# Optimization experiments

Measured on AMD Instinct MI355X. Metric: run time of the kernel, lower is better.

## Reference

```python
import jax, jax.numpy as jnp
import numpy as np

B, S, H = 4, 2048, 1024
NH, HD = 16, 64


def setup_inputs() -> dict:
    key = jax.random.key(0)
    ks = jax.random.split(key, 5)
    scale = 1.0 / np.sqrt(H)
    x = jax.random.normal(ks[0], (B, S, H), dtype=jnp.float32)
    w_qkv = jax.random.normal(ks[1], (H, 3 * H), dtype=jnp.float32) * scale
    b_qkv = jnp.zeros((3 * H,), dtype=jnp.float32)
    w_out = jax.random.normal(ks[2], (H, H), dtype=jnp.float32) * scale
    b_out = jnp.zeros((H,), dtype=jnp.float32)
    return {"x": x, "w_qkv": w_qkv, "b_qkv": b_qkv, "w_out": w_out, "b_out": b_out}


def reference(x, w_qkv, b_qkv, w_out, b_out):
    bsz, seq_len, hidden = x.shape
    qkv = x @ w_qkv + b_qkv  # [B,S,3H]
    q, k, v = jnp.split(qkv, 3, axis=-1)

    def heads(t):
        return t.reshape(bsz, seq_len, NH, HD).transpose(0, 2, 1, 3)  # [B,NH,S,HD]

    q, k, v = heads(q), heads(k), heads(v)
    scale = HD ** (-0.5)
    attn = jnp.einsum("bhqd,bhkd->bhqk", q, k) * scale  # [B,NH,S,S]
    causal = jnp.tril(jnp.ones((seq_len, seq_len), dtype=bool))
    attn = jnp.where(causal, attn, -jnp.inf)
    probs = jax.nn.softmax(attn, axis=-1)
    out = jnp.einsum("bhqk,bhkd->bhqd", probs, v)
    out = out.transpose(0, 2, 1, 3).reshape(bsz, seq_len, hidden)
    return out @ w_out + b_out
```

## Files before the change

### kernel.cpp

```cpp
#include <hip/hip_runtime.h>
#include <hip/hip_bf16.h>
#include <cstdint>

#define B_  4
#define S_  2048
#define H_  1024
#define NH_ 16
#define HD_ 64

using short8  = __attribute__((ext_vector_type(8))) short;
using floatx4 = __attribute__((ext_vector_type(4))) float;

__device__ __forceinline__ unsigned short f2b(float f) {
  union { float f; unsigned int u; } x; x.f = f;
  unsigned int r = x.u + 0x7fffu + ((x.u >> 16) & 1u);
  return (unsigned short)(r >> 16);
}
__device__ __forceinline__ unsigned short f2b_fast(float f) {
  union { float f; unsigned int u; } x; x.f = f;
  return (unsigned short)((x.u + 0x8000u) >> 16);
}
__device__ __forceinline__ unsigned int pack2(float a, float b) {
  return (unsigned int)f2b(a) | ((unsigned int)f2b(b) << 16);
}

__device__ __forceinline__ void async16(void* lds, const void* g) {
  __builtin_amdgcn_global_load_lds(
      (const __attribute__((address_space(1))) unsigned int*)g,
      (__attribute__((address_space(3))) unsigned int*)lds, 16, 0, 0);
}

__global__ void k_convert(const float* __restrict__ in, unsigned short* __restrict__ out, int n) {
  int i = (blockIdx.x * blockDim.x + threadIdx.x) * 4;
  if (i >= n) return;
  float4 v = *(const float4*)(in + i);
  ushort4 o;
  o.x = f2b(v.x); o.y = f2b(v.y); o.z = f2b(v.z); o.w = f2b(v.w);
  *(ushort4*)(out + i) = o;
}

__global__ void k_transpose_convert(const float* __restrict__ in, unsigned short* __restrict__ out,
                                    int R, int C) {
  __shared__ float tile[32][33];
  int tx = threadIdx.x & 31, ty = threadIdx.x >> 5;
  int c0 = blockIdx.x * 32, r0 = blockIdx.y * 32;
  for (int i = 0; i < 4; i++) {
    int r = r0 + ty + i * 8;
    tile[ty + i * 8][tx] = in[(size_t)r * C + c0 + tx];
  }
  __syncthreads();
  for (int i = 0; i < 4; i++) {
    int c = c0 + ty + i * 8;
    out[(size_t)c * R + r0 + tx] = f2b(tile[tx][ty + i * 8]);
  }
}

template <bool OUT_BF16>
__global__ __launch_bounds__(256, 2) void k_gemm_bt(
    const unsigned short* __restrict__ A,
    const unsigned short* __restrict__ BT,
    const float* __restrict__ bias,
    void* __restrict__ Cout,
    unsigned short* __restrict__ vt,
    int M, int N, int K) {
  __shared__ __align__(16) unsigned short As[2][128 * 64];
  __shared__ __align__(16) unsigned short Bs[2][128 * 64];
  const int tid  = threadIdx.x;
  const int lane = tid & 63, wave = tid >> 6;
  const int quad = lane >> 4, l16 = lane & 15;
  const int wm = wave >> 1, wn = wave & 1;
  const int m0 = blockIdx.y * 128, n0 = blockIdx.x * 128;
  const int wv2 = wave & 1;

  const unsigned short* srcbase = (wave < 2) ? A : BT;
  const int base0 = (wave < 2) ? m0 : n0;

  floatx4 acc[4][4];
  for (int mt = 0; mt < 4; mt++)
    for (int nt = 0; nt < 4; nt++)
      acc[mt][nt] = (floatx4){0.f, 0.f, 0.f, 0.f};

  auto stage = [&](int k0, int bufi) {
    unsigned short* dst = (wave < 2) ? &As[bufi][0] : &Bs[bufi][0];
    for (int j = 0; j < 8; j++) {
      int c = wv2 * 512 + j * 64 + lane;
      int row = c >> 3, slot = c & 7;
      int c8 = slot ^ (row & 7);
      async16(&dst[c * 8], &srcbase[(size_t)(base0 + row) * K + k0 + c8 * 8]);
    }
  };

  stage(0, 0);
  int it = 0;
  for (int k0 = 0; k0 < K; k0 += 64, it++) {
    const int cur = it & 1;
    __syncthreads();
    if (k0 + 64 < K) stage(k0 + 64, cur ^ 1);
    for (int kh = 0; kh < 2; kh++) {
      short8 af[4], bq[4];
      for (int t = 0; t < 4; t++) {
        int ra = wm * 64 + t * 16 + l16;
        int rb = wn * 64 + t * 16 + l16;
        af[t] = *(const short8*)&As[cur][(ra * 8 + ((kh * 4 + quad) ^ (ra & 7))) * 8];
        bq[t] = *(const short8*)&Bs[cur][(rb * 8 + ((kh * 4 + quad) ^ (rb & 7))) * 8];
      }
      for (int mt = 0; mt < 4; mt++)
        for (int nt = 0; nt < 4; nt++)
          acc[mt][nt] = __builtin_amdgcn_mfma_f32_16x16x32_bf16(af[mt], bq[nt], acc[mt][nt], 0, 0, 0);
    }
  }

  if (OUT_BF16 && n0 >= 2048) {
    for (int mt = 0; mt < 4; mt++) {
      int row0 = m0 + wm * 64 + mt * 16 + quad * 4;
      int b = row0 >> 11, s = row0 & 2047;
      for (int nt = 0; nt < 4; nt++) {
        int col = n0 + wn * 64 + nt * 16 + l16;
        float bv = bias[col];
        uint2 u;
        u.x = pack2(acc[mt][nt][0] + bv, acc[mt][nt][1] + bv);
        u.y = pack2(acc[mt][nt][2] + bv, acc[mt][nt][3] + bv);
        *(uint2*)&vt[(size_t)(b * 1024 + (col - 2048)) * S_ + s] = u;
      }
    }
  } else {
    for (int mt = 0; mt < 4; mt++) {
      int row = m0 + wm * 64 + mt * 16 + quad * 4;
      for (int nt = 0; nt < 4; nt++) {
        int col = n0 + wn * 64 + nt * 16 + l16;
        float bv = bias[col];
        for (int r = 0; r < 4; r++) {
          float v = acc[mt][nt][r] + bv;
          if (OUT_BF16) ((unsigned short*)Cout)[(size_t)(row + r) * N + col] = f2b(v);
          else          ((float*)Cout)[(size_t)(row + r) * N + col] = v;
        }
      }
    }
  }
}

__global__ __launch_bounds__(256, 3) void k_attn(
    const unsigned short* __restrict__ qkv,
    const unsigned short* __restrict__ vt,
    unsigned short* __restrict__ outb) {
  __shared__ __align__(16) unsigned short Ks [2][64 * 64];
  __shared__ __align__(16) unsigned short VTs[2][64 * 64];
  __shared__ __align__(16) unsigned short PsB[4][32][72];

  const int tid  = threadIdx.x;
  const int lane = tid & 63, w = tid >> 6;
  const int quad = lane >> 4, l16 = lane & 15;
  const int qt = gridDim.x - 1 - blockIdx.x;
  const int bh = blockIdx.y, b = bh >> 4, h = bh & 15;
  const int qwv = qt * 128 + w * 32;
  const int wv2 = w & 1;

  short8 qf[2][2];
  for (int g = 0; g < 2; g++)
    for (int kh = 0; kh < 2; kh++)
      qf[g][kh] = *(const short8*)&qkv[(size_t)(b * S_ + qwv + g * 16 + l16) * (3 * H_)
                                       + h * HD_ + kh * 32 + quad * 8];

  floatx4 oacc[2][4];
  float lsum[2] = {0.f, 0.f};
  for (int g = 0; g < 2; g++)
    for (int ct = 0; ct < 4; ct++) oacc[g][ct] = (floatx4){0.f, 0.f, 0.f, 0.f};

  auto stage = [&](int kt, int bufi) {
    if (w < 2) {
      for (int j = 0; j < 4; j++) {
        int c = wv2 * 256 + j * 64 + lane;
        int row = c >> 3, c8 = (c & 7) ^ (row & 7);
        async16(&Ks[bufi][c * 8],
                &qkv[(size_t)(b * S_ + kt * 64 + row) * (3 * H_) + H_ + h * HD_ + c8 * 8]);
      }
    } else {
      for (int j = 0; j < 4; j++) {
        int c = wv2 * 256 + j * 64 + lane;
        int row = c >> 3, c8 = (c & 7) ^ (row & 7);
        async16(&VTs[bufi][c * 8],
                &vt[(size_t)(bh * HD_ + row) * S_ + kt * 64 + c8 * 8]);
      }
    }
  };

  const int ktmax = 2 * qt + 1;
  stage(0, 0);
  for (int kt = 0; kt <= ktmax; kt++) {
    const int cur = kt & 1;
    __syncthreads();
    if (kt < ktmax) stage(kt + 1, cur ^ 1);

    if (kt * 64 <= qwv + 31) {
      const bool need_mask = (kt * 64 + 63 > qwv);

      short8 vf[4][2];
      for (int ct = 0; ct < 4; ct++)
        for (int kh = 0; kh < 2; kh++) {
          int vrow = ct * 16 + l16;
          vf[ct][kh] = *(const short8*)&VTs[cur][(vrow * 8 + ((kh * 4 + quad) ^ (vrow & 7))) * 8];
        }

      for (int ct = 0; ct < 4; ct++) {
        int krow = ct * 16 + l16;
        short8 kf0 = *(const short8*)&Ks[cur][(krow * 8 + ((0 + quad) ^ (krow & 7))) * 8];
        short8 kf1 = *(const short8*)&Ks[cur][(krow * 8 + ((4 + quad) ^ (krow & 7))) * 8];
        for (int g = 0; g < 2; g++) {
          floatx4 z = (floatx4){0.f, 0.f, 0.f, 0.f};
          z = __builtin_amdgcn_mfma_f32_16x16x32_bf16(kf0, qf[g][0], z, 0, 0, 0);
          z = __builtin_amdgcn_mfma_f32_16x16x32_bf16(kf1, qf[g][1], z, 0, 0, 0);
          float p[4];
          if (need_mask) {
            int kvb = kt * 64 + ct * 16 + quad * 4;
            int q = qwv + g * 16 + l16;
            for (int r = 0; r < 4; r++)
              p[r] = (kvb + r <= q) ? __expf(z[r] * 0.125f) : 0.f;
          } else {
            for (int r = 0; r < 4; r++) p[r] = __expf(z[r] * 0.125f);
          }
          lsum[g] += (p[0] + p[1]) + (p[2] + p[3]);
          uint2 u;
          u.x = (unsigned int)f2b_fast(p[0]) | ((unsigned int)f2b_fast(p[1]) << 16);
          u.y = (unsigned int)f2b_fast(p[2]) | ((unsigned int)f2b_fast(p[3]) << 16);
          *(uint2*)&PsB[w][g * 16 + l16][ct * 16 + quad * 4] = u;
        }
      }

      for (int g = 0; g < 2; g++)
        for (int kh = 0; kh < 2; kh++) {
          short8 pf = *(const short8*)&PsB[w][g * 16 + l16][kh * 32 + quad * 8];
          for (int ct = 0; ct < 4; ct++)
            oacc[g][ct] = __builtin_amdgcn_mfma_f32_16x16x32_bf16(vf[ct][kh], pf, oacc[g][ct], 0, 0, 0);
        }
    }
  }

  for (int g = 0; g < 2; g++) {
    lsum[g] += __shfl_xor(lsum[g], 16);
    lsum[g] += __shfl_xor(lsum[g], 32);
  }

  for (int g = 0; g < 2; g++) {
    float inv = 1.0f / lsum[g];
    int q = qwv + g * 16 + l16;
    for (int ct = 0; ct < 4; ct++) {
      uint2 u;
      u.x = pack2(oacc[g][ct][0] * inv, oacc[g][ct][1] * inv);
      u.y = pack2(oacc[g][ct][2] * inv, oacc[g][ct][3] * inv);
      *(uint2*)&outb[(size_t)(b * S_ + q) * H_ + h * HD_ + ct * 16 + quad * 4] = u;
    }
  }
}

extern "C" void kernel_launch(void* const* d_in, const int* in_sizes, int n_in,
                              void* d_out, int out_size, void* d_ws, size_t ws_size,
                              hipStream_t stream) {
  const float* x     = (const float*)d_in[0];
  const float* w_qkv = (const float*)d_in[1];
  const float* b_qkv = (const float*)d_in[2];
  const float* w_out = (const float*)d_in[3];
  const float* b_out = (const float*)d_in[4];

  char* ws = (char*)d_ws;
  size_t off = 0;
  auto alloc = [&](size_t bytes) -> void* {
    void* p = ws + off;
    off = (off + bytes + 255) & ~(size_t)255;
    return p;
  };
  unsigned short* xb    = (unsigned short*)alloc((size_t)B_ * S_ * H_ * 2);
  unsigned short* wqkvT = (unsigned short*)alloc((size_t)3 * H_ * H_ * 2);
  unsigned short* woutT = (unsigned short*)alloc((size_t)H_ * H_ * 2);
  unsigned short* qkv   = (unsigned short*)alloc((size_t)B_ * S_ * 3 * H_ * 2);
  unsigned short* ao    = (unsigned short*)alloc((size_t)B_ * S_ * H_ * 2);
  unsigned short* vtb   = (unsigned short*)alloc((size_t)B_ * NH_ * HD_ * S_ * 2);

  const int nx = B_ * S_ * H_;
  k_convert<<<nx / 4 / 256, 256, 0, stream>>>(x, xb, nx);
  k_transpose_convert<<<dim3(3 * H_ / 32, H_ / 32), 256, 0, stream>>>(w_qkv, wqkvT, H_, 3 * H_);
  k_transpose_convert<<<dim3(H_ / 32, H_ / 32), 256, 0, stream>>>(w_out, woutT, H_, H_);

  k_gemm_bt<true ><<<dim3(3 * H_ / 128, B_ * S_ / 128), 256, 0, stream>>>(
      xb, wqkvT, b_qkv, qkv, vtb, B_ * S_, 3 * H_, H_);

  k_attn<<<dim3(S_ / 128, B_ * NH_), 256, 0, stream>>>(qkv, vtb, ao);

  k_gemm_bt<false><<<dim3(H_ / 128, B_ * S_ / 128), 256, 0, stream>>>(
      ao, woutT, b_out, (float*)d_out, nullptr, B_ * S_, H_, H_);
}
```

Measured before the change: 299.5 us.

## Halve GEMM K-tile, shrink attention P buffer, and reorder attention grid by query tile

Result: slower. 371.8 us (+24.2%).

```diff
diff --git a/kernel.cpp b/kernel.cpp
--- a/kernel.cpp
+++ b/kernel.cpp
@@ -56,15 +56,15 @@
 }
 
 template <bool OUT_BF16>
-__global__ __launch_bounds__(256, 2) void k_gemm_bt(
+__global__ __launch_bounds__(256, 4) void k_gemm_bt(
     const unsigned short* __restrict__ A,
     const unsigned short* __restrict__ BT,
     const float* __restrict__ bias,
     void* __restrict__ Cout,
     unsigned short* __restrict__ vt,
     int M, int N, int K) {
-  __shared__ __align__(16) unsigned short As[2][128 * 64];
-  __shared__ __align__(16) unsigned short Bs[2][128 * 64];
+  __shared__ __align__(16) unsigned short As[2][128 * 32];
+  __shared__ __align__(16) unsigned short Bs[2][128 * 32];
   const int tid  = threadIdx.x;
   const int lane = tid & 63, wave = tid >> 6;
   const int quad = lane >> 4, l16 = lane & 15;
@@ -82,32 +82,30 @@
 
   auto stage = [&](int k0, int bufi) {
     unsigned short* dst = (wave < 2) ? &As[bufi][0] : &Bs[bufi][0];
-    for (int j = 0; j < 8; j++) {
-      int c = wv2 * 512 + j * 64 + lane;
-      int row = c >> 3, slot = c & 7;
-      int c8 = slot ^ (row & 7);
+    for (int j = 0; j < 4; j++) {
+      int c = wv2 * 256 + j * 64 + lane;
+      int row = c >> 2, slot = c & 3;
+      int c8 = slot ^ ((row >> 1) & 3);
       async16(&dst[c * 8], &srcbase[(size_t)(base0 + row) * K + k0 + c8 * 8]);
     }
   };
 
   stage(0, 0);
   int it = 0;
-  for (int k0 = 0; k0 < K; k0 += 64, it++) {
+  for (int k0 = 0; k0 < K; k0 += 32, it++) {
     const int cur = it & 1;
     __syncthreads();
-    if (k0 + 64 < K) stage(k0 + 64, cur ^ 1);
-    for (int kh = 0; kh < 2; kh++) {
-      short8 af[4], bq[4];
-      for (int t = 0; t < 4; t++) {
-        int ra = wm * 64 + t * 16 + l16;
-        int rb = wn * 64 + t * 16 + l16;
-        af[t] = *(const short8*)&As[cur][(ra * 8 + ((kh * 4 + quad) ^ (ra & 7))) * 8];
-        bq[t] = *(const short8*)&Bs[cur][(rb * 8 + ((kh * 4 + quad) ^ (rb & 7))) * 8];
-      }
-      for (int mt = 0; mt < 4; mt++)
-        for (int nt = 0; nt < 4; nt++)
-          acc[mt][nt] = __builtin_amdgcn_mfma_f32_16x16x32_bf16(af[mt], bq[nt], acc[mt][nt], 0, 0, 0);
-    }
+    if (k0 + 32 < K) stage(k0 + 32, cur ^ 1);
+    short8 af[4], bq[4];
+    for (int t = 0; t < 4; t++) {
+      int ra = wm * 64 + t * 16 + l16;
+      int rb = wn * 64 + t * 16 + l16;
+      af[t] = *(const short8*)&As[cur][(ra * 4 + (quad ^ ((ra >> 1) & 3))) * 8];
+      bq[t] = *(const short8*)&Bs[cur][(rb * 4 + (quad ^ ((rb >> 1) & 3))) * 8];
+    }
+    for (int mt = 0; mt < 4; mt++)
+      for (int nt = 0; nt < 4; nt++)
+        acc[mt][nt] = __builtin_amdgcn_mfma_f32_16x16x32_bf16(af[mt], bq[nt], acc[mt][nt], 0, 0, 0);
   }
 
   if (OUT_BF16 && n0 >= 2048) {
@@ -139,19 +137,20 @@
   }
 }
 
-__global__ __launch_bounds__(256, 3) void k_attn(
+__global__ __launch_bounds__(256, 4) void k_attn(
     const unsigned short* __restrict__ qkv,
     const unsigned short* __restrict__ vt,
     unsigned short* __restrict__ outb) {
   __shared__ __align__(16) unsigned short Ks [2][64 * 64];
   __shared__ __align__(16) unsigned short VTs[2][64 * 64];
-  __shared__ __align__(16) unsigned short PsB[4][32][72];
+  __shared__ __align__(16) unsigned short Ps[4][16 * 64];
 
   const int tid  = threadIdx.x;
   const int lane = tid & 63, w = tid >> 6;
   const int quad = lane >> 4, l16 = lane & 15;
-  const int qt = gridDim.x - 1 - blockIdx.x;
-  const int bh = blockIdx.y, b = bh >> 4, h = bh & 15;
+  const int qt = (S_ / 128 - 1) - (blockIdx.x >> 6);
+  const int bh = blockIdx.x & 63;
+  const int b = bh >> 4, h = bh & 15;
   const int qwv = qt * 128 + w * 32;
   const int wv2 = w & 1;
 
@@ -184,6 +183,8 @@
     }
   };
 
+  unsigned short* Pw = &Ps[w][0];
+
   const int ktmax = 2 * qt + 1;
   stage(0, 0);
   for (int kt = 0; kt <= ktmax; kt++) {
@@ -201,6 +202,7 @@
           vf[ct][kh] = *(const short8*)&VTs[cur][(vrow * 8 + ((kh * 4 + quad) ^ (vrow & 7))) * 8];
         }
 
+      uint2 pk[2][4];
       for (int ct = 0; ct < 4; ct++) {
         int krow = ct * 16 + l16;
         short8 kf0 = *(const short8*)&Ks[cur][(krow * 8 + ((0 + quad) ^ (krow & 7))) * 8];
@@ -219,19 +221,22 @@
             for (int r = 0; r < 4; r++) p[r] = __expf(z[r] * 0.125f);
           }
           lsum[g] += (p[0] + p[1]) + (p[2] + p[3]);
-          uint2 u;
-          u.x = (unsigned int)f2b_fast(p[0]) | ((unsigned int)f2b_fast(p[1]) << 16);
-          u.y = (unsigned int)f2b_fast(p[2]) | ((unsigned int)f2b_fast(p[3]) << 16);
-          *(uint2*)&PsB[w][g * 16 + l16][ct * 16 + quad * 4] = u;
-        }
-      }
-
-      for (int g = 0; g < 2; g++)
+          pk[g][ct].x = (unsigned int)f2b_fast(p[0]) | ((unsigned int)f2b_fast(p[1]) << 16);
+          pk[g][ct].y = (unsigned int)f2b_fast(p[2]) | ((unsigned int)f2b_fast(p[3]) << 16);
+        }
+      }
+
+      for (int g = 0; g < 2; g++) {
+        for (int ct = 0; ct < 4; ct++) {
+          int slot = (ct * 2 + (quad >> 1)) ^ (l16 & 7);
+          *(uint2*)&Pw[l16 * 64 + slot * 8 + (quad & 1) * 4] = pk[g][ct];
+        }
         for (int kh = 0; kh < 2; kh++) {
-          short8 pf = *(const short8*)&PsB[w][g * 16 + l16][kh * 32 + quad * 8];
+          short8 pf = *(const short8*)&Pw[l16 * 64 + ((kh * 4 + quad) ^ (l16 & 7)) * 8];
           for (int ct = 0; ct < 4; ct++)
             oacc[g][ct] = __builtin_amdgcn_mfma_f32_16x16x32_bf16(vf[ct][kh], pf, oacc[g][ct], 0, 0, 0);
         }
+      }
     }
   }
 
@@ -283,7 +288,7 @@
   k_gemm_bt<true ><<<dim3(3 * H_ / 128, B_ * S_ / 128), 256, 0, stream>>>(
       xb, wqkvT, b_qkv, qkv, vtb, B_ * S_, 3 * H_, H_);
 
-  k_attn<<<dim3(S_ / 128, B_ * NH_), 256, 0, stream>>>(qkv, vtb, ao);
+  k_attn<<<(S_ / 128) * 64, 256, 0, stream>>>(qkv, vtb, ao);
 
   k_gemm_bt<false><<<dim3(H_ / 128, B_ * S_ / 128), 256, 0, stream>>>(
       ao, woutT, b_out, (float*)d_out, nullptr, B_ * S_, H_, H_);
```
